# Kernel tuning notes

Measured on AMD Instinct MI355X. Metric: run time of the kernel, lower is better.

## Reference

```python
import jax, jax.numpy as jnp
import numpy as np
import math

NUM_BITS = 8
EPS = 1e-5


def fake_quant(x, num_bits=NUM_BITS):
    """Uniform fake quantization over the tensor's full range (min/max), STE-friendly."""
    qmax = 2.0 ** num_bits - 1.0
    mn = jnp.min(x)
    mx = jnp.max(x)
    scale = jnp.maximum((mx - mn) / qmax, 1e-8)
    q = jnp.round(jnp.clip((x - mn) / scale, 0.0, qmax)) * scale + mn
    # straight-through estimator: forward = q, backward = identity
    return x + jax.lax.stop_gradient(q - x)


def qconv(x, w, stride, pad):
    """QConv2d: fake-quantize input (8b) and weight (8b), then fp conv (no bias)."""
    return jax.lax.conv_general_dilated(
        fake_quant(x), fake_quant(w),
        window_strides=(stride, stride),
        padding=[(pad, pad), (pad, pad)],
        dimension_numbers=("NCHW", "OIHW", "NCHW"))


def range_norm(x, gamma, beta):
    """RangeN / RangeBN (Banner et al.): per-channel mean subtraction and
    range-based scale (max-min over N,H,W) with the Gaussian range correction
    factor; affine params with 8-bit fake-quantized gamma."""
    B, C, H, W = x.shape
    n = B * H * W  # elements per channel
    scale_fix = (0.5 * 0.35) * (1.0 + (math.pi * math.log(4.0)) ** 0.5) / ((2.0 * math.log(n)) ** 0.5)
    mean = jnp.mean(x, axis=(0, 2, 3), keepdims=True)          # [1,C,1,1]
    xc = x - mean
    rng = jnp.max(xc, axis=(0, 2, 3), keepdims=True) - jnp.min(xc, axis=(0, 2, 3), keepdims=True)
    out = xc / (rng * scale_fix + EPS)
    qg = fake_quant(gamma)
    return out * qg[None, :, None, None] + beta[None, :, None, None]


def qsum(a, b):
    """Qsum: fake-quantize both addends to 8 bits, then add."""
    return fake_quant(a) + fake_quant(b)


def setup_inputs() -> dict:
    key = jax.random.key(0)
    ks = jax.random.split(key, 4)
    B, Cin, H, W = 64, 1024, 14, 14
    P = 256  # planes; expansion 4 -> Cout = 1024 == Cin (identity residual)
    x = jax.random.normal(ks[0], (B, Cin, H, W), jnp.float32)
    w1 = jax.random.normal(ks[1], (P, Cin, 1, 1), jnp.float32) * (1.0 / math.sqrt(Cin))
    w2 = jax.random.normal(ks[2], (P, P, 3, 3), jnp.float32) * (1.0 / math.sqrt(P * 9))
    w3 = jax.random.normal(ks[3], (4 * P, P, 1, 1), jnp.float32) * (1.0 / math.sqrt(P))
    g1 = jnp.ones((P,), jnp.float32); b1 = jnp.zeros((P,), jnp.float32)
    g2 = jnp.ones((P,), jnp.float32); b2 = jnp.zeros((P,), jnp.float32)
    g3 = jnp.ones((4 * P,), jnp.float32); b3 = jnp.zeros((4 * P,), jnp.float32)
    return {"x": x, "w1": w1, "g1": g1, "b1": b1, "w2": w2, "g2": g2, "b2": b2,
            "w3": w3, "g3": g3, "b3": b3}


def reference(x, w1, g1, b1, w2, g2, b2, w3, g3, b3):
    out = qconv(x, w1, stride=1, pad=0)
    out = range_norm(out, g1, b1)
    out = qconv(out, w2, stride=1, pad=1)
    out = range_norm(out, g2, b2)
    out = qconv(out, w3, stride=1, pad=0)
    out = range_norm(out, g3, b3)
    return qsum(x, out)  # downsample is None -> identity residual
```

## Files before the change

kernel.cpp:

```cpp
#include <hip/hip_runtime.h>
#include <math.h>

#ifndef M_PI
#define M_PI 3.14159265358979323846
#endif

#define NB   64
#define NCOL 12544

typedef __attribute__((ext_vector_type(4))) int int4v;

static const size_t OF_OUT = 0;
static const size_t OF_XC  = 3211264;
static const size_t OF_Z1P = 6422528;
static const size_t OF_Z2C = 7471104;
static const size_t OF_WQ1 = 8273920;
static const size_t OF_WQ2 = 8339456;
static const size_t OF_WQ3 = 8486912;
static const size_t OF_R1  = 8552448;
static const size_t OF_R2  = 8552704;
static const size_t OF_R3  = 8552960;
static const size_t OF_T2  = 8553984;
static const size_t OF_CX  = 8556032;
static const size_t OF_U2  = 8568576;
static const size_t OF_CZ  = 8597504;
static const size_t OF_SD1 = 8610048;
static const size_t OF_SD2 = 8610560;
static const size_t OF_SD3 = 8611072;
static const size_t OF_MN1 = 8613120;
static const size_t OF_MX1 = 8613376;
static const size_t OF_MN2 = 8613632;
static const size_t OF_MX2 = 8613888;
static const size_t OF_MN3 = 8614144;
static const size_t OF_MX3 = 8615168;
static const size_t OF_PMM = 9061632;
static const size_t OF_ST  = 9068800;

__device__ __forceinline__ float fqv(float v, float mn, float sc) {
    float t = (v - mn) / sc;
    t = fminf(fmaxf(t, 0.0f), 255.0f);
    return rintf(t) * sc + mn;
}
__device__ __forceinline__ float codef(float v, float mn, float sc) {
    float t = (v - mn) / sc;
    t = fminf(fmaxf(t, 0.0f), 255.0f);
    return rintf(t) - 128.0f;
}
__device__ __forceinline__ unsigned short f2bf(float f) { return (unsigned short)(__float_as_uint(f) >> 16); }
__device__ __forceinline__ float bf2f(unsigned short u) { return __uint_as_float(((unsigned)u) << 16); }
__device__ __forceinline__ int pack4(float a, float b, float c, float d) {
    return (int)(unsigned char)(signed char)(int)a | ((int)(unsigned char)(signed char)(int)b << 8) |
           ((int)(unsigned char)(signed char)(int)c << 16) | ((int)(unsigned char)(signed char)(int)d << 24);
}
__device__ __forceinline__ void glds16(const void* g, void* l) {
    __builtin_amdgcn_global_load_lds((const __attribute__((address_space(1))) unsigned int*)g,
                                     (__attribute__((address_space(3))) unsigned int*)l, 16, 0, 0);
}
__device__ __forceinline__ unsigned fkey(float f) {
    unsigned u = __float_as_uint(f);
    return (u & 0x80000000u) ? ~u : (u | 0x80000000u);
}
__device__ __forceinline__ float unfkey(unsigned k) {
    unsigned u = (k & 0x80000000u) ? (k & 0x7FFFFFFFu) : ~k;
    return __uint_as_float(u);
}

__device__ __forceinline__ void blk_minmax(float& mn, float& mx, volatile float* scr) {
    for (int o = 32; o; o >>= 1) {
        mn = fminf(mn, __shfl_down(mn, o, 64));
        mx = fmaxf(mx, __shfl_down(mx, o, 64));
    }
    int lane = threadIdx.x & 63, wv = threadIdx.x >> 6;
    __syncthreads();
    if (lane == 0) { scr[wv] = mn; scr[4 + wv] = mx; }
    __syncthreads();
    mn = fminf(fminf(scr[0], scr[1]), fminf(scr[2], scr[3]));
    mx = fmaxf(fmaxf(scr[4], scr[5]), fmaxf(scr[6], scr[7]));
}

template <int C>
__device__ void stage_params(const float* __restrict__ gamma, const float* __restrict__ beta,
                             const double* __restrict__ sumd, const unsigned* __restrict__ mnk,
                             const unsigned* __restrict__ mxk, float scale_fix,
                             float* lmean, float* lsg, volatile float* scr,
                             float& zmn, float& zsc) {
    int t = threadIdx.x;
    float gmn = INFINITY, gmx = -INFINITY;
    for (int c = t; c < C; c += 256) {
        float g = gamma[c];
        gmn = fminf(gmn, g); gmx = fmaxf(gmx, g);
    }
    blk_minmax(gmn, gmx, scr);
    float gsc = fmaxf((gmx - gmn) / 255.0f, 1e-8f);
    float qmn = INFINITY, qmx = -INFINITY;
    for (int c = t; c < C; c += 256) {
        float mean = (float)sumd[c] / 12544.0f;
        float cmn = unfkey(mnk[c]), cmx = unfkey(mxk[c]);
        float rng = cmx - cmn;
        float qg = fqv(gamma[c], gmn, gsc);
        float s = qg / (rng * scale_fix + 1e-5f);
        if (lmean) { lmean[c] = mean; lsg[c] = s; }
        float b = beta[c];
        float lo = (cmn - mean) * s + b;
        float hi = (cmx - mean) * s + b;
        qmn = fminf(qmn, fminf(lo, hi));
        qmx = fmaxf(qmx, fmaxf(lo, hi));
    }
    blk_minmax(qmn, qmx, scr);
    zmn = qmn;
    zsc = fmaxf((qmx - qmn) / 255.0f, 1e-8f);
}

__global__ __launch_bounds__(256) void k_minmax_all(const float4* __restrict__ x, const float4* __restrict__ w1,
                                                    const float4* __restrict__ w2, const float4* __restrict__ w3,
                                                    float* __restrict__ Pmm, float* __restrict__ Wf) {
    {
        unsigned g = blockIdx.x * 256 + threadIdx.x;
        int* zp = (int*)(Wf + OF_Z1P);
        for (unsigned i = g; i < 1048576u; i += 327680u) zp[i] = 0;
        if (g < 12544u) Wf[OF_CX + g] = 0.0f;
        if (g < 16384u) Wf[OF_U2 + g] = 0.0f;
        if (g < 3072u)  ((int*)(Wf + OF_SD1))[g] = 0;
        if (g < 256u) {
            ((unsigned*)(Wf + OF_MN1))[g] = 0xFF800000u;
            ((unsigned*)(Wf + OF_MX1))[g] = 0x007FFFFFu;
            ((unsigned*)(Wf + OF_MN2))[g] = 0xFF800000u;
            ((unsigned*)(Wf + OF_MX2))[g] = 0x007FFFFFu;
        }
        if (g < 1024u) {
            ((unsigned*)(Wf + OF_MN3))[g] = 0xFF800000u;
            ((unsigned*)(Wf + OF_MX3))[g] = 0x007FFFFFu;
        }
    }
    int b = blockIdx.x;
    const float4* p; int lb, nb, n4, base;
    if (b < 1024)      { p = x;  lb = b;        nb = 1024; n4 = 3211264; base = 0; }
    else if (b < 1088) { p = w1; lb = b - 1024; nb = 64;   n4 = 65536;   base = 2048; }
    else if (b < 1216) { p = w2; lb = b - 1088; nb = 128;  n4 = 147456;  base = 2176; }
    else               { p = w3; lb = b - 1216; nb = 64;   n4 = 65536;   base = 2432; }
    float mn = INFINITY, mx = -INFINITY;
    for (int i = lb * 256 + threadIdx.x; i < n4; i += nb * 256) {
        float4 v = p[i];
        mn = fminf(mn, fminf(fminf(v.x, v.y), fminf(v.z, v.w)));
        mx = fmaxf(mx, fmaxf(fmaxf(v.x, v.y), fmaxf(v.z, v.w)));
    }
    for (int o = 32; o; o >>= 1) {
        mn = fminf(mn, __shfl_down(mn, o, 64));
        mx = fmaxf(mx, __shfl_down(mx, o, 64));
    }
    __shared__ float smn[4], smx[4];
    int lane = threadIdx.x & 63, w = threadIdx.x >> 6;
    if (lane == 0) { smn[w] = mn; smx[w] = mx; }
    __syncthreads();
    if (threadIdx.x == 0) {
        for (int i = 1; i < 4; i++) { mn = fminf(mn, smn[i]); mx = fmaxf(mx, smx[i]); }
        Pmm[base + lb * 2]     = mn;
        Pmm[base + lb * 2 + 1] = mx;
    }
}

__global__ __launch_bounds__(256) void k_fqparams2(const float* __restrict__ Pmm, float* __restrict__ sf) {
    __shared__ float sa[4], sb[4];
    int t = threadIdx.x, lane = t & 63, w = t >> 6;
    const int nbs[4]   = {1024, 64, 128, 64};
    const int bases[4] = {0, 2048, 2176, 2432};
    for (int ten = 0; ten < 4; ten++) {
        float mn = INFINITY, mx = -INFINITY;
        for (int i = t; i < nbs[ten]; i += 256) {
            mn = fminf(mn, Pmm[bases[ten] + 2 * i]);
            mx = fmaxf(mx, Pmm[bases[ten] + 2 * i + 1]);
        }
        for (int o = 32; o; o >>= 1) {
            mn = fminf(mn, __shfl_down(mn, o, 64));
            mx = fmaxf(mx, __shfl_down(mx, o, 64));
        }
        if (lane == 0) { sa[w] = mn; sb[w] = mx; }
        __syncthreads();
        if (t == 0) {
            mn = fminf(fminf(sa[0], sa[1]), fminf(sa[2], sa[3]));
            mx = fmaxf(fmaxf(sb[0], sb[1]), fmaxf(sb[2], sb[3]));
            sf[8 + 3 * ten] = mn;
            sf[9 + 3 * ten] = fmaxf((mx - mn) / 255.0f, 1e-8f);
        }
        __syncthreads();
    }
}

__global__ __launch_bounds__(256) void k_prep(const float* __restrict__ x, signed char* __restrict__ xdst,
                                              const float* __restrict__ sf, float* __restrict__ CX,
                                              const float* __restrict__ w1, const float* __restrict__ w2,
                                              const float* __restrict__ w3,
                                              signed char* __restrict__ wq1, signed char* __restrict__ wq2,
                                              signed char* __restrict__ wq3,
                                              float* __restrict__ R1, float* __restrict__ R2,
                                              float* __restrict__ R3, float* __restrict__ T8) {
    int t = threadIdx.x;
    int lane = t & 63, wv = t >> 6;
    if (blockIdx.x < 1792) {
        __shared__ unsigned short lt[28][264];
        int u = blockIdx.x;
        int n = u / 28, r = u - n * 28;
        int hw0 = (r % 7) * 28, cq = (r / 7) * 256;
        float qmn = sf[8], qsc = sf[9];
        const float* sp = x + ((size_t)n * 1024 + cq) * 196 + hw0;
        for (int i = t; i < 7168; i += 256) {
            int c = i / 28, hw = i - c * 28;
            lt[hw][c] = f2bf(codef(sp[(size_t)c * 196 + hw], qmn, qsc));
        }
        __syncthreads();
        int c0 = lane * 4;
#pragma unroll
        for (int s = 0; s < 7; s++) {
            int i = s * 4 + wv;
            int pk = pack4(bf2f(lt[i][c0]), bf2f(lt[i][c0 + 1]), bf2f(lt[i][c0 + 2]), bf2f(lt[i][c0 + 3]));
            *(int*)&xdst[((size_t)n * 196 + hw0 + i) * 1024 + cq + c0] = pk;
        }
        for (int i = wv; i < 28; i += 4) {
            float s = bf2f(lt[i][lane]) + bf2f(lt[i][lane + 64]) +
                      bf2f(lt[i][lane + 128]) + bf2f(lt[i][lane + 192]);
            for (int o = 32; o; o >>= 1) s += __shfl_down(s, o, 64);
            if (lane == 0) atomicAdd(&CX[n * 196 + hw0 + i], s);
        }
        return;
    }
    __shared__ float sh[64];
    int b = blockIdx.x - 1792;
    if (b < 1280) {
        const float* w; signed char* wc; float* R; int K, co; const float* pw;
        if (b < 256) { w = w1; wc = wq1; R = R1; K = 1024; co = b; pw = sf + 11; }
        else         { w = w3; wc = wq3; R = R3; K = 256;  co = b - 256; pw = sf + 17; }
        float mn = pw[0], s = pw[1];
        float sum = 0.f;
        for (int k0 = t * 4; k0 < K; k0 += 1024) {
            float4 v = *(const float4*)&w[(size_t)co * K + k0];
            float c0 = codef(v.x, mn, s), c1 = codef(v.y, mn, s), c2 = codef(v.z, mn, s), c3 = codef(v.w, mn, s);
            *(int*)&wc[(size_t)co * K + k0] = pack4(c0, c1, c2, c3);
            sum += c0 + c1 + c2 + c3;
        }
        for (int o = 32; o; o >>= 1) sum += __shfl_down(sum, o, 64);
        if (lane == 0) sh[wv] = sum;
        __syncthreads();
        if (t == 0) R[co] = sh[0] + sh[1] + sh[2] + sh[3];
    } else {
        int co = b - 1280, ci = t;
        float mn = sf[14], s = sf[15];
        float tp[9];
#pragma unroll
        for (int p = 0; p < 9; p++) {
            float c = codef(w2[((size_t)co * 256 + ci) * 9 + p], mn, s);
            wq2[(size_t)co * 2304 + p * 256 + ci] = (signed char)(int)c;
            tp[p] = c;
        }
        float* red = sh;
        float* sT = sh + 40;
#pragma unroll
        for (int p = 0; p < 9; p++) {
            float v = tp[p];
            for (int o = 32; o; o >>= 1) v += __shfl_down(v, o, 64);
            if (lane == 0) red[wv * 9 + p] = v;
        }
        __syncthreads();
        if (ci < 9) sT[ci] = red[ci] + red[9 + ci] + red[18 + ci] + red[27 + ci];
        __syncthreads();
        if (ci == 0) {
            float T0 = sT[0], T1 = sT[1], T2 = sT[2], T3 = sT[3],
                  T5 = sT[5], T6 = sT[6], T7 = sT[7], T8v = sT[8];
            R2[co] = T0 + T1 + T2 + T3 + sT[4] + T5 + T6 + T7 + T8v;
            float* o = &T8[co * 8];
            o[0] = T0 + T1 + T2;
            o[1] = T6 + T7 + T8v;
            o[2] = T0 + T3 + T6;
            o[3] = T2 + T5 + T8v;
            o[4] = T0; o[5] = T2; o[6] = T6; o[7] = T8v;
        }
    }
}

template <int PAD>
__global__ __launch_bounds__(256) void k_codeE(const float* __restrict__ src, signed char* __restrict__ dst,
                                               const float* __restrict__ gamma, const float* __restrict__ beta_g,
                                               const double* __restrict__ sumd, const unsigned* __restrict__ mnk,
                                               const unsigned* __restrict__ mxk, float scale_fix,
                                               float* __restrict__ rowsum) {
    __shared__ __align__(16) float lmean[256];
    __shared__ __align__(16) float lsg[256];
    __shared__ float scr[8];
    float qmn, qsc;
    stage_params<256>(gamma, beta_g, sumd, mnk, mxk, scale_fix, lmean, lsg, scr, qmn, qsc);
    __syncthreads();
    int t = threadIdx.x, lane = t & 63, wv = t >> 6;
    int c4 = lane * 4;
    float4 m4 = *(const float4*)&lmean[c4];
    float4 s4 = *(const float4*)&lsg[c4];
    float4 b4 = *(const float4*)&beta_g[c4];
#pragma unroll
    for (int r = 0; r < 4; r++) {
        int j = blockIdx.x * 16 + wv * 4 + r;
        float4 v = *(const float4*)&src[(size_t)j * 256 + c4];
        float c0 = codef((v.x - m4.x) * s4.x + b4.x, qmn, qsc);
        float c1 = codef((v.y - m4.y) * s4.y + b4.y, qmn, qsc);
        float c2 = codef((v.z - m4.z) * s4.z + b4.z, qmn, qsc);
        float c3 = codef((v.w - m4.w) * s4.w + b4.w, qmn, qsc);
        int n = j / 196, hw = j - n * 196, h = hw / 14, w = hw - (hw / 14) * 14;
        size_t di;
        if (PAD) di = (((size_t)n * 16 + h + 1) * 16 + (w + 1)) * 256 + c4;
        else     di = (size_t)j * 256 + c4;
        *(int*)&dst[di] = pack4(c0, c1, c2, c3);
        float s = c0 + c1 + c2 + c3;
        for (int o = 32; o; o >>= 1) s += __shfl_down(s, o, 64);
        if (lane == 0) {
            if (PAD) rowsum[((size_t)n * 16 + h + 1) * 16 + (w + 1)] = s;
            else     rowsum[j] = s;
        }
    }
}

template <int MODE>
__global__ __launch_bounds__(256, 2) void k_conv12(const signed char* __restrict__ Acts,
                                                   const signed char* __restrict__ Wts,
                                                   const float* __restrict__ R, const float* __restrict__ T8,
                                                   const float* __restrict__ Cj,
                                                   const float* __restrict__ pw, const float* __restrict__ pz,
                                                   const float* __restrict__ pzg, const float* __restrict__ pzb,
                                                   const double* __restrict__ pzsum,
                                                   const unsigned* __restrict__ pzmn,
                                                   const unsigned* __restrict__ pzmx, float scale_fix,
                                                   float* __restrict__ outNHWC, int K,
                                                   double* __restrict__ Sumd, unsigned* __restrict__ Mnk,
                                                   unsigned* __restrict__ Mxk) {
    __shared__ __align__(16) signed char As[2 * 16384];
    __shared__ __align__(16) signed char Bs[2 * 8192];
    __shared__ float Lst[2][64][3];
    __shared__ float pscr[8];
    __shared__ float Vl[128];
    int tid = threadIdx.x, lane = tid & 63, wave = tid >> 6;
    int wm = wave >> 1, wn = wave & 1;
    int bid = blockIdx.x;
    int xcd = bid & 7, slot = bid >> 3;
    int tile = xcd * 49 + slot;
    int jb = (tile >> 2) * 128, cob = (tile & 3) * 64;
    int sr = tid >> 3, spos = tid & 7, sc = spos ^ (sr & 7);

    const signed char* aq[4];
#pragma unroll
    for (int q = 0; q < 4; q++) {
        int j = jb + q * 32 + sr;
        if (MODE == 0) aq[q] = Acts + (size_t)j * K + sc * 16;
        else {
            int n = j / 196, hw = j - n * 196, h = hw / 14, w = hw - (hw / 14) * 14;
            aq[q] = Acts + (((size_t)n * 16 + h) * 16 + w) * 256 + sc * 16;
        }
    }
    const signed char* bq[2];
#pragma unroll
    for (int q = 0; q < 2; q++) bq[q] = Wts + (size_t)(cob + q * 32 + sr) * K + sc * 16;

    int nk = K >> 7;
    auto stage = [&](int b, int ks) {
        size_t koA;
        if (MODE == 0) koA = (size_t)ks << 7;
        else {
            int k = ks << 7;
            int p = k >> 8, kin = k & 255;
            int rr = p / 3, ss = p - 3 * rr;
            koA = (size_t)(rr * 16 + ss) * 256 + kin;
        }
#pragma unroll
        for (int q = 0; q < 4; q++)
            glds16(aq[q] + koA, &As[b * 16384 + (q * 32 + sr) * 128 + spos * 16]);
#pragma unroll
        for (int q = 0; q < 2; q++)
            glds16(bq[q] + ((size_t)ks << 7), &Bs[b * 8192 + (q * 32 + sr) * 128 + spos * 16]);
    };

    stage(0, 0);
    float zmn = 0.f, zsc = 0.f;
    if (MODE == 1) {
        stage_params<256>(pzg, pzb, pzsum, pzmn, pzmx, scale_fix, nullptr, nullptr, pscr, zmn, zsc);
        if (tid < 128) {
            int j = jb + tid;
            int n_ = j / 196, hw_ = j - n_ * 196, h_ = hw_ / 14, w_ = hw_ - (hw_ / 14) * 14;
            const float* u = Cj + n_ * 256 + h_ * 16 + w_;
            Vl[tid] = u[0] + u[1] + u[2] + u[16] + u[17] + u[18] + u[32] + u[33] + u[34];
        }
    }

    int4v acc[4][2];
#pragma unroll
    for (int mi = 0; mi < 4; mi++)
#pragma unroll
        for (int ni = 0; ni < 2; ni++) acc[mi][ni] = (int4v)0;

    int l15 = lane & 15, kq = lane >> 4, sw = l15 & 7;
    for (int ks = 0; ks < nk; ks++) {
        __syncthreads();
        if (ks + 1 < nk) stage((ks + 1) & 1, ks + 1);
        int b = ks & 1;
#pragma unroll
        for (int kc = 0; kc < 2; kc++) {
            int col = ((kc * 4 + kq) ^ sw) << 4;
            int4v a[4], bb[2];
#pragma unroll
            for (int mi = 0; mi < 4; mi++)
                a[mi] = *(const int4v*)&As[b * 16384 + (wm * 64 + mi * 16 + l15) * 128 + col];
#pragma unroll
            for (int ni = 0; ni < 2; ni++)
                bb[ni] = *(const int4v*)&Bs[b * 8192 + (wn * 32 + ni * 16 + l15) * 128 + col];
#pragma unroll
            for (int mi = 0; mi < 4; mi++)
#pragma unroll
                for (int ni = 0; ni < 2; ni++)
                    acc[mi][ni] = __builtin_amdgcn_mfma_i32_16x16x64_i8(a[mi], bb[ni], acc[mi][ni], 0, 0, 0);
        }
    }

    float aw = pw[1], bw = pw[0] + 128.f * pw[1];
    float az, bz;
    if (MODE == 1) { az = zsc; bz = zmn + 128.f * zsc; }
    else           { az = pz[1]; bz = pz[0] + 128.f * pz[1]; }
    float caa = aw * az, cR = aw * bz, cC = bw * az, cK = bw * bz;
    int cco[2]; float rr0[2]; float t8v[2][8];
#pragma unroll
    for (int ni = 0; ni < 2; ni++) {
        cco[ni] = cob + wn * 32 + ni * 16 + l15;
        rr0[ni] = R[cco[ni]];
        if (MODE == 1) {
#pragma unroll
            for (int p = 0; p < 8; p++) t8v[ni][p] = T8[cco[ni] * 8 + p];
        }
    }
    float ssm[2] = {0.f, 0.f}, smnv[2] = {INFINITY, INFINITY}, smxv[2] = {-INFINITY, -INFINITY};
#pragma unroll
    for (int mi = 0; mi < 4; mi++)
#pragma unroll
        for (int reg = 0; reg < 4; reg++) {
            int j = jb + wm * 64 + mi * 16 + kq * 4 + reg;
            int n = j / 196, hw = j - n * 196;
            float constterm, cjv;
            float pt = 0.f, pb = 0.f, pl = 0.f, pr = 0.f, ctl = 0.f, ctr = 0.f, cbl = 0.f, cbr = 0.f;
            if (MODE == 1) {
                int h = hw / 14, w = hw - (hw / 14) * 14;
                pt = (h == 0) ? 1.f : 0.f;  pb = (h == 13) ? 1.f : 0.f;
                pl = (w == 0) ? 1.f : 0.f;  pr = (w == 13) ? 1.f : 0.f;
                ctl = pt * pl; ctr = pt * pr; cbl = pb * pl; cbr = pb * pr;
                float miss = 3.f * (pt + pb + pl + pr) - (ctl + ctr + cbl + cbr);
                constterm = cK * (256.f * (9.f - miss));
                cjv = Vl[j - jb];
            } else {
                constterm = cK * (float)K;
                cjv = Cj[j];
            }
#pragma unroll
            for (int ni = 0; ni < 2; ni++) {
                float rsum = rr0[ni];
                if (MODE == 1)
                    rsum -= pt * t8v[ni][0] + pb * t8v[ni][1] + pl * t8v[ni][2] + pr * t8v[ni][3]
                          - ctl * t8v[ni][4] - ctr * t8v[ni][5] - cbl * t8v[ni][6] - cbr * t8v[ni][7];
                float v = caa * (float)acc[mi][ni][reg] + cR * rsum + cC * cjv + constterm;
                outNHWC[(size_t)j * 256 + cco[ni]] = v;
                ssm[ni] += v;
                smnv[ni] = fminf(smnv[ni], v);
                smxv[ni] = fmaxf(smxv[ni], v);
            }
        }
#pragma unroll
    for (int ni = 0; ni < 2; ni++) {
        float s = ssm[ni], mn = smnv[ni], mx = smxv[ni];
        s += __shfl_xor(s, 16, 64); s += __shfl_xor(s, 32, 64);
        mn = fminf(mn, __shfl_xor(mn, 16, 64)); mn = fminf(mn, __shfl_xor(mn, 32, 64));
        mx = fmaxf(mx, __shfl_xor(mx, 16, 64)); mx = fmaxf(mx, __shfl_xor(mx, 32, 64));
        if (kq == 0) {
            int cl = wn * 32 + ni * 16 + l15;
            Lst[wm][cl][0] = s; Lst[wm][cl][1] = mn; Lst[wm][cl][2] = mx;
        }
    }
    __syncthreads();
    if (tid < 64) {
        float s  = Lst[0][tid][0] + Lst[1][tid][0];
        float mn = fminf(Lst[0][tid][1], Lst[1][tid][1]);
        float mx = fmaxf(Lst[0][tid][2], Lst[1][tid][2]);
        int co = cob + tid;
        atomicAdd(&Sumd[co], (double)s);
        atomicMin(&Mnk[co], fkey(mn));
        atomicMax(&Mxk[co], fkey(mx));
    }
}

__global__ __launch_bounds__(256, 2) void k_conv3(const signed char* __restrict__ Wts,
                                                  const signed char* __restrict__ Zc,
                                                  const float* __restrict__ R, const float* __restrict__ Cj,
                                                  const float* __restrict__ pw,
                                                  const float* __restrict__ pzg, const float* __restrict__ pzb,
                                                  const double* __restrict__ pzsum,
                                                  const unsigned* __restrict__ pzmn,
                                                  const unsigned* __restrict__ pzmx, float scale_fix,
                                                  float* __restrict__ out,
                                                  double* __restrict__ Sumd, unsigned* __restrict__ Mnk,
                                                  unsigned* __restrict__ Mxk) {
    __shared__ __align__(16) signed char As[32768];
    __shared__ __align__(16) signed char Bs[32768];
    __shared__ float Lst[2][128][3];
    __shared__ float pscr[8];
    int tid = threadIdx.x, lane = tid & 63, wave = tid >> 6;
    int wm = wave >> 1, wn = wave & 1;
    int bid = blockIdx.x;
    int xcd = bid & 7, slot = bid >> 3;
    int tile = xcd * 98 + slot;
    int jb = (tile >> 3) * 128, cob = (tile & 7) * 128;
    int sr = tid >> 4, spos = tid & 15;

#pragma unroll
    for (int p = 0; p < 8; p++) {
        int row = p * 16 + sr;
        int cg = spos ^ (row & 7);
        glds16(Zc + (size_t)(jb + row) * 256 + cg * 16, &As[p * 4096 + tid * 16]);
    }
#pragma unroll
    for (int p = 0; p < 8; p++) {
        int row = p * 16 + sr;
        int cg = spos ^ (row & 7);
        glds16(Wts + (size_t)(cob + row) * 256 + cg * 16, &Bs[p * 4096 + tid * 16]);
    }

    float zmn, zsc;
    stage_params<256>(pzg, pzb, pzsum, pzmn, pzmx, scale_fix, nullptr, nullptr, pscr, zmn, zsc);
    __syncthreads();

    int4v acc[4][4];
#pragma unroll
    for (int mi = 0; mi < 4; mi++)
#pragma unroll
        for (int ni = 0; ni < 4; ni++) acc[mi][ni] = (int4v)0;

    int l15 = lane & 15, kq = lane >> 4, sw = l15 & 7;
#pragma unroll
    for (int kc = 0; kc < 4; kc++) {
        int col = ((kc * 4 + kq) ^ sw) << 4;
        int4v a[4], bb[4];
#pragma unroll
        for (int mi = 0; mi < 4; mi++)
            a[mi] = *(const int4v*)&As[(wm * 64 + mi * 16 + l15) * 256 + col];
#pragma unroll
        for (int ni = 0; ni < 4; ni++)
            bb[ni] = *(const int4v*)&Bs[(wn * 64 + ni * 16 + l15) * 256 + col];
#pragma unroll
        for (int mi = 0; mi < 4; mi++)
#pragma unroll
            for (int ni = 0; ni < 4; ni++)
                acc[mi][ni] = __builtin_amdgcn_mfma_i32_16x16x64_i8(a[mi], bb[ni], acc[mi][ni], 0, 0, 0);
    }

    float aw = pw[1], bw = pw[0] + 128.f * pw[1];
    float az = zsc, bz = zmn + 128.f * zsc;
    float caa = aw * az, cR = aw * bz, cC = bw * az, cK = bw * bz;
    int coA[4]; float rA[4];
#pragma unroll
    for (int ni = 0; ni < 4; ni++) {
        coA[ni] = cob + wn * 64 + ni * 16 + l15;
        rA[ni] = R[coA[ni]];
    }
    float ps[4], pmn[4], pmx[4];
#pragma unroll
    for (int ni = 0; ni < 4; ni++) { ps[ni] = 0.f; pmn[ni] = INFINITY; pmx[ni] = -INFINITY; }
#pragma unroll
    for (int mi = 0; mi < 4; mi++) {
        int j0 = jb + wm * 64 + mi * 16 + kq * 4;
        int n = j0 / 196, hh = j0 - n * 196;
        float4 cj = *(const float4*)&Cj[j0];
#pragma unroll
        for (int ni = 0; ni < 4; ni++) {
            float base = cR * rA[ni] + cK * 256.f;
            float4 v;
            v.x = caa * (float)acc[mi][ni][0] + base + cC * cj.x;
            v.y = caa * (float)acc[mi][ni][1] + base + cC * cj.y;
            v.z = caa * (float)acc[mi][ni][2] + base + cC * cj.z;
            v.w = caa * (float)acc[mi][ni][3] + base + cC * cj.w;
            *(float4*)&out[((size_t)n * 1024 + coA[ni]) * 196 + hh] = v;
            ps[ni] += v.x + v.y + v.z + v.w;
            pmn[ni] = fminf(pmn[ni], fminf(fminf(v.x, v.y), fminf(v.z, v.w)));
            pmx[ni] = fmaxf(pmx[ni], fmaxf(fmaxf(v.x, v.y), fmaxf(v.z, v.w)));
        }
    }
#pragma unroll
    for (int ni = 0; ni < 4; ni++) {
        float s = ps[ni], mn = pmn[ni], mx = pmx[ni];
        s += __shfl_xor(s, 16, 64); s += __shfl_xor(s, 32, 64);
        mn = fminf(mn, __shfl_xor(mn, 16, 64)); mn = fminf(mn, __shfl_xor(mn, 32, 64));
        mx = fmaxf(mx, __shfl_xor(mx, 16, 64)); mx = fmaxf(mx, __shfl_xor(mx, 32, 64));
        if (kq == 0) {
            int cl = wn * 64 + ni * 16 + l15;
            Lst[wm][cl][0] = s; Lst[wm][cl][1] = mn; Lst[wm][cl][2] = mx;
        }
    }
    __syncthreads();
    if (tid < 128) {
        float s  = Lst[0][tid][0] + Lst[1][tid][0];
        float mn = fminf(Lst[0][tid][1], Lst[1][tid][1]);
        float mx = fmaxf(Lst[0][tid][2], Lst[1][tid][2]);
        int co = cob + tid;
        atomicAdd(&Sumd[co], (double)s);
        atomicMin(&Mnk[co], fkey(mn));
        atomicMax(&Mxk[co], fkey(mx));
    }
}

__global__ __launch_bounds__(256) void k_final(const signed char* __restrict__ xc, float* __restrict__ out,
                                               const float* __restrict__ gamma, const float* __restrict__ beta,
                                               const double* __restrict__ sumd, const unsigned* __restrict__ mnk,
                                               const unsigned* __restrict__ mxk, float scale_fix,
                                               const float* __restrict__ sf) {
    __shared__ __align__(16) signed char lx[196 * 68 + 4];
    __shared__ float lmean[1024];
    __shared__ float lsg[1024];
    __shared__ float scr[8];
    int t = threadIdx.x;
    int n = blockIdx.x >> 4, cg = blockIdx.x & 15;
    const signed char* xp = xc + (size_t)n * 200704 + cg * 64;
    for (int i = t; i < 3136; i += 256) {
        int row = i >> 4, col = i & 15;
        int v = *(const int*)(xp + (size_t)row * 1024 + col * 4);
        *(int*)&lx[row * 68 + col * 4] = v;
    }
    float qmn, qsc;
    stage_params<1024>(gamma, beta, sumd, mnk, mxk, scale_fix, lmean, lsg, scr, qmn, qsc);
    __syncthreads();
    float xmn = sf[8], xsc = sf[9];
    float xoff = xmn + 128.f * xsc;
    float4* op = (float4*)(out + ((size_t)n * 1024 + cg * 64) * 196);
    for (int idx = t; idx < 3136; idx += 256) {
        int c = idx / 49, f = idx - c * 49;
        int hw = f * 4;
        float4 ov = op[idx];
        int cc = cg * 64 + c;
        float m = lmean[cc], s = lsg[cc], b = beta[cc];
        const signed char* lr = &lx[hw * 68 + c];
        float4 r;
        r.x = (float)lr[0]   * xsc + xoff + fqv((ov.x - m) * s + b, qmn, qsc);
        r.y = (float)lr[68]  * xsc + xoff + fqv((ov.y - m) * s + b, qmn, qsc);
        r.z = (float)lr[136] * xsc + xoff + fqv((ov.z - m) * s + b, qmn, qsc);
        r.w = (float)lr[204] * xsc + xoff + fqv((ov.w - m) * s + b, qmn, qsc);
        op[idx] = r;
    }
}

extern "C" void kernel_launch(void* const* d_in, const int* in_sizes, int n_in,
                              void* d_out, int out_size, void* d_ws, size_t ws_size,
                              hipStream_t stream) {
    const float* x  = (const float*)d_in[0];
    const float* w1 = (const float*)d_in[1];
    const float* g1 = (const float*)d_in[2];
    const float* b1 = (const float*)d_in[3];
    const float* w2 = (const float*)d_in[4];
    const float* g2 = (const float*)d_in[5];
    const float* b2 = (const float*)d_in[6];
    const float* w3 = (const float*)d_in[7];
    const float* g3 = (const float*)d_in[8];
    const float* b3 = (const float*)d_in[9];
    float* out = (float*)d_out;

    float* W = (float*)d_ws;
    float* OUT = W + OF_OUT;
    signed char* xc  = (signed char*)(W + OF_XC);
    signed char* z1p = (signed char*)(W + OF_Z1P);
    signed char* z2c = (signed char*)(W + OF_Z2C);
    signed char* wq1 = (signed char*)(W + OF_WQ1);
    signed char* wq2 = (signed char*)(W + OF_WQ2);
    signed char* wq3 = (signed char*)(W + OF_WQ3);
    float* R1 = W + OF_R1; float* R2 = W + OF_R2; float* R3 = W + OF_R3;
    float* T2 = W + OF_T2;
    float* CX = W + OF_CX; float* U2 = W + OF_U2; float* CZ = W + OF_CZ;
    double* SD1 = (double*)(W + OF_SD1);
    double* SD2 = (double*)(W + OF_SD2);
    double* SD3 = (double*)(W + OF_SD3);
    unsigned* MN1 = (unsigned*)(W + OF_MN1); unsigned* MX1 = (unsigned*)(W + OF_MX1);
    unsigned* MN2 = (unsigned*)(W + OF_MN2); unsigned* MX2 = (unsigned*)(W + OF_MX2);
    unsigned* MN3 = (unsigned*)(W + OF_MN3); unsigned* MX3 = (unsigned*)(W + OF_MX3);
    float* Pmm = W + OF_PMM;
    float* S = W + OF_ST;

    const float scale_fix =
        (float)((0.5 * 0.35) * (1.0 + sqrt(M_PI * log(4.0))) / sqrt(2.0 * log(12544.0)));

    k_minmax_all<<<1280, 256, 0, stream>>>((const float4*)x, (const float4*)w1,
                                           (const float4*)w2, (const float4*)w3, Pmm, W);
    k_fqparams2<<<1, 256, 0, stream>>>(Pmm, S);

    k_prep<<<3328, 256, 0, stream>>>(x, xc, S, CX, w1, w2, w3, wq1, wq2, wq3, R1, R2, R3, T2);

    k_conv12<0><<<392, 256, 0, stream>>>(xc, wq1, R1, nullptr, CX, S + 11, S + 8,
                                         nullptr, nullptr, nullptr, nullptr, nullptr, 0.f,
                                         OUT, 1024, SD1, MN1, MX1);
    k_codeE<1><<<784, 256, 0, stream>>>(OUT, z1p, g1, b1, SD1, MN1, MX1, scale_fix, U2);

    k_conv12<1><<<392, 256, 0, stream>>>(z1p, wq2, R2, T2, U2, S + 14, nullptr,
                                         g1, b1, SD1, MN1, MX1, scale_fix,
                                         OUT, 2304, SD2, MN2, MX2);
    k_codeE<0><<<784, 256, 0, stream>>>(OUT, z2c, g2, b2, SD2, MN2, MX2, scale_fix, CZ);

    k_conv3<<<784, 256, 0, stream>>>(wq3, z2c, R3, CZ, S + 17,
                                     g2, b2, SD2, MN2, MX2, scale_fix,
                                     out, SD3, MN3, MX3);

    k_final<<<1024, 256, 0, stream>>>(xc, out, g3, b3, SD3, MN3, MX3, scale_fix, S);
}
```

Before: 238.4 us.

## Fuse stage-2 normalize/quantize into conv3 and fold fq-params into prep

Removes the k_codeE<0> pass by having k_conv3 read the fp32 conv2 output directly, apply range-norm affine and fake-quant codes in the prologue, write int8 tiles into LDS, and compute per-row code sums locally. Also drops the single-block k_fqparams2 launch: each k_prep block derives its quantization params from the partial min/max buffer itself, and one extra block writes the params still needed by later kernels. This saves two launches and an int8 round trip through memory, at the cost of redundant reductions in every prep block and a slower, non-async fp32 load prologue in conv3 that can no longer overlap the A-tile fetch.

```diff
diff --git a/kernel.cpp b/kernel.cpp
--- a/kernel.cpp
+++ b/kernel.cpp
@@ -13,7 +13,6 @@
 static const size_t OF_OUT = 0;
 static const size_t OF_XC  = 3211264;
 static const size_t OF_Z1P = 6422528;
-static const size_t OF_Z2C = 7471104;
 static const size_t OF_WQ1 = 8273920;
 static const size_t OF_WQ2 = 8339456;
 static const size_t OF_WQ3 = 8486912;
@@ -23,7 +22,6 @@
 static const size_t OF_T2  = 8553984;
 static const size_t OF_CX  = 8556032;
 static const size_t OF_U2  = 8568576;
-static const size_t OF_CZ  = 8597504;
 static const size_t OF_SD1 = 8610048;
 static const size_t OF_SD2 = 8610560;
 static const size_t OF_SD3 = 8611072;
@@ -76,6 +74,18 @@
     __syncthreads();
     mn = fminf(fminf(scr[0], scr[1]), fminf(scr[2], scr[3]));
     mx = fmaxf(fmaxf(scr[4], scr[5]), fmaxf(scr[6], scr[7]));
+}
+
+__device__ __forceinline__ void derive_fq(const float* __restrict__ Pmm, int base, int nb,
+                                          volatile float* scr, float& mn_o, float& sc_o) {
+    float mn = INFINITY, mx = -INFINITY;
+    for (int i = threadIdx.x; i < nb; i += 256) {
+        mn = fminf(mn, Pmm[base + 2 * i]);
+        mx = fmaxf(mx, Pmm[base + 2 * i + 1]);
+    }
+    blk_minmax(mn, mx, scr);
+    mn_o = mn;
+    sc_o = fmaxf((mx - mn) / 255.0f, 1e-8f);
 }
 
 template <int C>
@@ -159,49 +169,51 @@
     }
 }
 
-__global__ __launch_bounds__(256) void k_fqparams2(const float* __restrict__ Pmm, float* __restrict__ sf) {
-    __shared__ float sa[4], sb[4];
-    int t = threadIdx.x, lane = t & 63, w = t >> 6;
-    const int nbs[4]   = {1024, 64, 128, 64};
-    const int bases[4] = {0, 2048, 2176, 2432};
-    for (int ten = 0; ten < 4; ten++) {
-        float mn = INFINITY, mx = -INFINITY;
-        for (int i = t; i < nbs[ten]; i += 256) {
-            mn = fminf(mn, Pmm[bases[ten] + 2 * i]);
-            mx = fmaxf(mx, Pmm[bases[ten] + 2 * i + 1]);
-        }
-        for (int o = 32; o; o >>= 1) {
-            mn = fminf(mn, __shfl_down(mn, o, 64));
-            mx = fmaxf(mx, __shfl_down(mx, o, 64));
-        }
-        if (lane == 0) { sa[w] = mn; sb[w] = mx; }
-        __syncthreads();
-        if (t == 0) {
-            mn = fminf(fminf(sa[0], sa[1]), fminf(sa[2], sa[3]));
-            mx = fmaxf(fmaxf(sb[0], sb[1]), fmaxf(sb[2], sb[3]));
-            sf[8 + 3 * ten] = mn;
-            sf[9 + 3 * ten] = fmaxf((mx - mn) / 255.0f, 1e-8f);
-        }
-        __syncthreads();
-    }
-}
-
 __global__ __launch_bounds__(256) void k_prep(const float* __restrict__ x, signed char* __restrict__ xdst,
-                                              const float* __restrict__ sf, float* __restrict__ CX,
+                                              const float* __restrict__ Pmm, float* __restrict__ sf,
+                                              float* __restrict__ CX,
                                               const float* __restrict__ w1, const float* __restrict__ w2,
                                               const float* __restrict__ w3,
                                               signed char* __restrict__ wq1, signed char* __restrict__ wq2,
                                               signed char* __restrict__ wq3,
                                               float* __restrict__ R1, float* __restrict__ R2,
                                               float* __restrict__ R3, float* __restrict__ T8) {
+    __shared__ float scr8[8];
     int t = threadIdx.x;
     int lane = t & 63, wv = t >> 6;
+    if (blockIdx.x == 3328) {
+        __shared__ float sa[4], sb[4];
+        const int nbs[4]   = {1024, 64, 128, 64};
+        const int bases[4] = {0, 2048, 2176, 2432};
+        for (int ten = 0; ten < 4; ten++) {
+            float mn = INFINITY, mx = -INFINITY;
+            for (int i = t; i < nbs[ten]; i += 256) {
+                mn = fminf(mn, Pmm[bases[ten] + 2 * i]);
+                mx = fmaxf(mx, Pmm[bases[ten] + 2 * i + 1]);
+            }
+            for (int o = 32; o; o >>= 1) {
+                mn = fminf(mn, __shfl_down(mn, o, 64));
+                mx = fmaxf(mx, __shfl_down(mx, o, 64));
+            }
+            if (lane == 0) { sa[wv] = mn; sb[wv] = mx; }
+            __syncthreads();
+            if (t == 0) {
+                mn = fminf(fminf(sa[0], sa[1]), fminf(sa[2], sa[3]));
+                mx = fmaxf(fmaxf(sb[0], sb[1]), fmaxf(sb[2], sb[3]));
+                sf[8 + 3 * ten] = mn;
+                sf[9 + 3 * ten] = fmaxf((mx - mn) / 255.0f, 1e-8f);
+            }
+            __syncthreads();
+        }
+        return;
+    }
     if (blockIdx.x < 1792) {
+        float qmn, qsc;
+        derive_fq(Pmm, 0, 1024, scr8, qmn, qsc);
         __shared__ unsigned short lt[28][264];
         int u = blockIdx.x;
         int n = u / 28, r = u - n * 28;
         int hw0 = (r % 7) * 28, cq = (r / 7) * 256;
-        float qmn = sf[8], qsc = sf[9];
         const float* sp = x + ((size_t)n * 1024 + cq) * 196 + hw0;
         for (int i = t; i < 7168; i += 256) {
             int c = i / 28, hw = i - c * 28;
@@ -226,10 +238,10 @@
     __shared__ float sh[64];
     int b = blockIdx.x - 1792;
     if (b < 1280) {
-        const float* w; signed char* wc; float* R; int K, co; const float* pw;
-        if (b < 256) { w = w1; wc = wq1; R = R1; K = 1024; co = b; pw = sf + 11; }
-        else         { w = w3; wc = wq3; R = R3; K = 256;  co = b - 256; pw = sf + 17; }
-        float mn = pw[0], s = pw[1];
+        const float* w; signed char* wc; float* R; int K, co;
+        float mn, s;
+        if (b < 256) { w = w1; wc = wq1; R = R1; K = 1024; co = b;       derive_fq(Pmm, 2048, 64, scr8, mn, s); }
+        else         { w = w3; wc = wq3; R = R3; K = 256;  co = b - 256; derive_fq(Pmm, 2432, 64, scr8, mn, s); }
         float sum = 0.f;
         for (int k0 = t * 4; k0 < K; k0 += 1024) {
             float4 v = *(const float4*)&w[(size_t)co * K + k0];
@@ -242,8 +254,9 @@
         __syncthreads();
         if (t == 0) R[co] = sh[0] + sh[1] + sh[2] + sh[3];
     } else {
+        float mn, s;
+        derive_fq(Pmm, 2176, 128, scr8, mn, s);
         int co = b - 1280, ci = t;
-        float mn = sf[14], s = sf[15];
         float tp[9];
 #pragma unroll
         for (int p = 0; p < 9; p++) {
@@ -487,8 +500,8 @@
 }
 
 __global__ __launch_bounds__(256, 2) void k_conv3(const signed char* __restrict__ Wts,
-                                                  const signed char* __restrict__ Zc,
-                                                  const float* __restrict__ R, const float* __restrict__ Cj,
+                                                  const float* __restrict__ Osrc,
+                                                  const float* __restrict__ R,
                                                   const float* __restrict__ pw,
                                                   const float* __restrict__ pzg, const float* __restrict__ pzb,
                                                   const double* __restrict__ pzsum,
@@ -501,6 +514,10 @@
     __shared__ __align__(16) signed char Bs[32768];
     __shared__ float Lst[2][128][3];
     __shared__ float pscr[8];
+    __shared__ __align__(16) float lmean[256];
+    __shared__ __align__(16) float lsg[256];
+    __shared__ __align__(16) float lbeta[256];
+    __shared__ __align__(16) float CjL[128];
     int tid = threadIdx.x, lane = tid & 63, wave = tid >> 6;
     int wm = wave >> 1, wn = wave & 1;
     int bid = blockIdx.x;
@@ -513,17 +530,31 @@
     for (int p = 0; p < 8; p++) {
         int row = p * 16 + sr;
         int cg = spos ^ (row & 7);
-        glds16(Zc + (size_t)(jb + row) * 256 + cg * 16, &As[p * 4096 + tid * 16]);
-    }
-#pragma unroll
-    for (int p = 0; p < 8; p++) {
-        int row = p * 16 + sr;
-        int cg = spos ^ (row & 7);
         glds16(Wts + (size_t)(cob + row) * 256 + cg * 16, &Bs[p * 4096 + tid * 16]);
     }
+    lbeta[tid] = pzb[tid];
 
     float zmn, zsc;
-    stage_params<256>(pzg, pzb, pzsum, pzmn, pzmx, scale_fix, nullptr, nullptr, pscr, zmn, zsc);
+    stage_params<256>(pzg, pzb, pzsum, pzmn, pzmx, scale_fix, lmean, lsg, pscr, zmn, zsc);
+
+    {
+        int g = lane >> 2;
+        int sub = (lane & 3) << 2;
+        for (int k = 0; k < 32; k++) {
+            int r = k * 4 + wave;
+            const float* orow = Osrc + (size_t)(jb + r) * 256 + lane * 4;
+            float4 v = *(const float4*)orow;
+            int c0 = lane * 4;
+            float q0 = codef((v.x - lmean[c0])     * lsg[c0]     + lbeta[c0],     zmn, zsc);
+            float q1 = codef((v.y - lmean[c0 + 1]) * lsg[c0 + 1] + lbeta[c0 + 1], zmn, zsc);
+            float q2 = codef((v.z - lmean[c0 + 2]) * lsg[c0 + 2] + lbeta[c0 + 2], zmn, zsc);
+            float q3 = codef((v.w - lmean[c0 + 3]) * lsg[c0 + 3] + lbeta[c0 + 3], zmn, zsc);
+            *(int*)&As[r * 256 + ((g ^ (r & 7)) << 4) + sub] = pack4(q0, q1, q2, q3);
+            float s = q0 + q1 + q2 + q3;
+            for (int o = 32; o; o >>= 1) s += __shfl_down(s, o, 64);
+            if (lane == 0) CjL[r] = s;
+        }
+    }
     __syncthreads();
 
     int4v acc[4][4];
@@ -566,7 +597,7 @@
     for (int mi = 0; mi < 4; mi++) {
         int j0 = jb + wm * 64 + mi * 16 + kq * 4;
         int n = j0 / 196, hh = j0 - n * 196;
-        float4 cj = *(const float4*)&Cj[j0];
+        float4 cj = *(const float4*)&CjL[wm * 64 + mi * 16 + kq * 4];
 #pragma unroll
         for (int ni = 0; ni < 4; ni++) {
             float base = cR * rA[ni] + cK * 256.f;
@@ -662,13 +693,12 @@
     float* OUT = W + OF_OUT;
     signed char* xc  = (signed char*)(W + OF_XC);
     signed char* z1p = (signed char*)(W + OF_Z1P);
-    signed char* z2c = (signed char*)(W + OF_Z2C);
     signed char* wq1 = (signed char*)(W + OF_WQ1);
     signed char* wq2 = (signed char*)(W + OF_WQ2);
     signed char* wq3 = (signed char*)(W + OF_WQ3);
     float* R1 = W + OF_R1; float* R2 = W + OF_R2; float* R3 = W + OF_R3;
     float* T2 = W + OF_T2;
-    float* CX = W + OF_CX; float* U2 = W + OF_U2; float* CZ = W + OF_CZ;
+    float* CX = W + OF_CX; float* U2 = W + OF_U2;
     double* SD1 = (double*)(W + OF_SD1);
     double* SD2 = (double*)(W + OF_SD2);
     double* SD3 = (double*)(W + OF_SD3);
@@ -683,9 +713,8 @@
 
     k_minmax_all<<<1280, 256, 0, stream>>>((const float4*)x, (const float4*)w1,
                                            (const float4*)w2, (const float4*)w3, Pmm, W);
-    k_fqparams2<<<1, 256, 0, stream>>>(Pmm, S);
-
-    k_prep<<<3328, 256, 0, stream>>>(x, xc, S, CX, w1, w2, w3, wq1, wq2, wq3, R1, R2, R3, T2);
+
+    k_prep<<<3329, 256, 0, stream>>>(x, xc, Pmm, S, CX, w1, w2, w3, wq1, wq2, wq3, R1, R2, R3, T2);
 
     k_conv12<0><<<392, 256, 0, stream>>>(xc, wq1, R1, nullptr, CX, S + 11, S + 8,
                                          nullptr, nullptr, nullptr, nullptr, nullptr, 0.f,
@@ -695,9 +724,8 @@
     k_conv12<1><<<392, 256, 0, stream>>>(z1p, wq2, R2, T2, U2, S + 14, nullptr,
                                          g1, b1, SD1, MN1, MX1, scale_fix,
                                          OUT, 2304, SD2, MN2, MX2);
-    k_codeE<0><<<784, 256, 0, stream>>>(OUT, z2c, g2, b2, SD2, MN2, MX2, scale_fix, CZ);
-
-    k_conv3<<<784, 256, 0, stream>>>(wq3, z2c, R3, CZ, S + 17,
+
+    k_conv3<<<784, 256, 0, stream>>>(wq3, OUT, R3, S + 17,
                                      g2, b2, SD2, MN2, MX2, scale_fix,
                                      out, SD3, MN3, MX3);
 
```

Measured after the change: 263.1 us. 10.4% more time.
